# Kernel tuning notes

Measured on AMD Instinct MI355X. Metric: run time of the kernel, lower is better.

## Reference

```python
import jax, jax.numpy as jnp
import numpy as np
from jax import lax

EPS = 1e-5

def conv3x3(x, w):
    # NCHW conv, stride 1, padding 1, no bias
    return lax.conv_general_dilated(x, w, window_strides=(1, 1),
                                    padding=((1, 1), (1, 1)),
                                    dimension_numbers=('NCHW', 'OIHW', 'NCHW'))

def bn_train(x, gamma, beta):
    # training-mode BatchNorm2d: batch stats over (N,H,W), biased variance
    mean = jnp.mean(x, axis=(0, 2, 3), keepdims=True)
    var = jnp.mean((x - mean) ** 2, axis=(0, 2, 3), keepdims=True)
    xn = (x - mean) * lax.rsqrt(var + EPS)
    return xn * gamma[None, :, None, None] + beta[None, :, None, None]

def maxpool2(x):
    return lax.reduce_window(x, -jnp.inf, lax.max, (1, 1, 2, 2), (1, 1, 2, 2), 'VALID')

def decomposed_layer(x, dfe_w, dse_g, dse_b, dse_w, bn_g, bn_b):
    # DFE: conv without bias
    x_dfe = conv3x3(x, dfe_w)                     # [B, T, H, W]
    # DSE vectorized: per-channel BN(1)+ReLU == per-channel BN over T, then
    # 1x1 conv 1->G per channel == scalar expand; concat == interleave (i*G+g)
    xr = jax.nn.relu(bn_train(x_dfe, dse_g, dse_b))
    B, T, H, W = xr.shape
    G = dse_w.shape[1]
    x_dse = jnp.einsum('bihw,ig->bighw', xr, dse_w).reshape(B, T * G, H, W)
    # DFE's BN + ReLU
    return jax.nn.relu(bn_train(x_dse, bn_g, bn_b))

def setup_inputs() -> dict:
    key = jax.random.key(0)
    ks = jax.random.split(key, 12)
    B, G = 4096, 2
    d = {}
    d['x'] = jax.random.normal(ks[0], (B, 3, 32, 32), dtype=jnp.float32)
    # layer 1: T_dfe = ceil(16/2) = 8
    d['dfe1_w'] = jax.random.normal(ks[1], (8, 3, 3, 3), dtype=jnp.float32) * 0.1
    d['dse1_g'] = jnp.ones((8,), jnp.float32)
    d['dse1_b'] = jnp.zeros((8,), jnp.float32)
    d['dse1_w'] = jax.random.normal(ks[2], (8, G), dtype=jnp.float32) * 0.3
    d['bn1_g'] = jnp.ones((16,), jnp.float32)
    d['bn1_b'] = jnp.zeros((16,), jnp.float32)
    # layer 2: T_dfe = ceil(32/2) = 16
    d['dfe2_w'] = jax.random.normal(ks[3], (16, 16, 3, 3), dtype=jnp.float32) * 0.1
    d['dse2_g'] = jnp.ones((16,), jnp.float32)
    d['dse2_b'] = jnp.zeros((16,), jnp.float32)
    d['dse2_w'] = jax.random.normal(ks[4], (16, G), dtype=jnp.float32) * 0.3
    d['bn2_g'] = jnp.ones((32,), jnp.float32)
    d['bn2_b'] = jnp.zeros((32,), jnp.float32)
    # FC head
    d['fc1_w'] = jax.random.normal(ks[5], (512, 32 * 8 * 8), dtype=jnp.float32) * 0.02
    d['fc1_b'] = jnp.zeros((512,), jnp.float32)
    d['fc2_w'] = jax.random.normal(ks[6], (512, 512), dtype=jnp.float32) * 0.04
    d['fc2_b'] = jnp.zeros((512,), jnp.float32)
    d['fc3_w'] = jax.random.normal(ks[7], (10, 512), dtype=jnp.float32) * 0.04
    d['fc3_b'] = jnp.zeros((10,), jnp.float32)
    return d

def reference(x, dfe1_w, dse1_g, dse1_b, dse1_w, bn1_g, bn1_b,
              dfe2_w, dse2_g, dse2_b, dse2_w, bn2_g, bn2_b,
              fc1_w, fc1_b, fc2_w, fc2_b, fc3_w, fc3_b):
    h = decomposed_layer(x, dfe1_w, dse1_g, dse1_b, dse1_w, bn1_g, bn1_b)   # [B,16,32,32]
    h = maxpool2(h)                                                          # [B,16,16,16]
    h = decomposed_layer(h, dfe2_w, dse2_g, dse2_b, dse2_w, bn2_g, bn2_b)   # [B,32,16,16]
    h = maxpool2(h)                                                          # [B,32,8,8]
    h = h.reshape(h.shape[0], -1)                                            # [B,2048]
    h = jax.nn.relu(h @ fc1_w.T + fc1_b)
    h = jax.nn.relu(h @ fc2_w.T + fc2_b)
    return h @ fc3_w.T + fc3_b                                               # [B,10]
```

## Files before the change

kernel.cpp:

```cpp
#include <hip/hip_runtime.h>
#include <math.h>

#define EPS_BN 1e-5

namespace {

constexpr double CNT1 = 4096.0 * 1024.0;
constexpr double CNT2 = 4096.0 * 256.0;

constexpr size_t OFF_Y1 = 0;
constexpr size_t OFF_Y2 = 67108864;
constexpr size_t OFF_H2 = 100663296;
constexpr size_t OFF_A1 = 117440512;
constexpr size_t OFF_A2 = 121634816;
constexpr size_t OFF_ST = 134217728;
constexpr size_t OFF_WB1 = 134283264;
constexpr size_t OFF_WB2 = 136380416;

#define STG(p, i) (p)[(size_t)(i) * 8]

typedef short bf16x8 __attribute__((ext_vector_type(8)));
typedef float f32x4 __attribute__((ext_vector_type(4)));
typedef _Float16 f16;
typedef _Float16 f16x2 __attribute__((ext_vector_type(2)));
typedef _Float16 f16x4 __attribute__((ext_vector_type(4)));
typedef _Float16 f16x8 __attribute__((ext_vector_type(8)));

__device__ __forceinline__ short f2bf(float f) {
  unsigned u = __float_as_uint(f);
  u = (u + 0x7fffu + ((u >> 16) & 1u)) >> 16;
  return (short)u;
}

__device__ __forceinline__ void block_stats_lds(const float* s, const float* q,
                                                float* __restrict__ sred,
                                                double* __restrict__ st) {
  const int tid = threadIdx.x;
#pragma unroll
  for (int j = 0; j < 8; ++j) {
    sred[j * 257 + tid] = s[j];
    sred[(j + 8) * 257 + tid] = q[j];
  }
  __syncthreads();
  const int row = tid >> 4, seg = tid & 15;
  float p = 0.f;
#pragma unroll
  for (int k = 0; k < 16; ++k) {
    const int ke = (k + seg) & 15;
    p += sred[row * 257 + seg * 16 + ke];
  }
  p += __shfl_down(p, 8, 64);
  p += __shfl_down(p, 4, 64);
  p += __shfl_down(p, 2, 64);
  p += __shfl_down(p, 1, 64);
  if (seg == 0) {
    const int c = (row < 8) ? row : row - 8;
    const int slot = (row < 8) ? 2 * c : 2 * c + 1;
    unsafeAtomicAdd(st + (size_t)slot * 8, (double)p);
  }
}

__device__ __forceinline__ float wave_sum(float v) {
#pragma unroll
  for (int o = 32; o > 0; o >>= 1) v += __shfl_down(v, o, 64);
  return v;
}

__global__ __launch_bounds__(256) void k_conv1_y1(
    const float* __restrict__ x, const float* __restrict__ w1,
    f16* __restrict__ y1, double* __restrict__ st1) {
  __shared__ __align__(16) float smem[16 * 257];
  float* xs = smem;
  float* wk = smem + 3672;
  const int tid = threadIdx.x;
  if (tid < 216) wk[(tid % 27) * 8 + tid / 27] = w1[tid];
  const float* xp = x + (size_t)blockIdx.x * 3072;
  for (int i = tid; i < 600; i += 256) {
    const int ci = i / 200, rem = i - ci * 200;
    int r, c;
    if (rem < 36) { r = 0; c = rem; }
    else if (rem < 72) { r = 33; c = rem - 36; }
    else { const int j = rem - 72; r = 1 + (j >> 2); const int m = j & 3;
           c = (m == 0) ? 0 : 32 + m; }
    xs[ci * 1224 + r * 36 + c] = 0.f;
  }
  for (int i = tid; i < 3072; i += 256) {
    const int ci = i >> 10, r = (i >> 5) & 31, c = i & 31;
    xs[ci * 1224 + (r + 1) * 36 + (c + 1)] = xp[i];
  }
  const int rr = tid >> 3, c0 = (tid & 7) * 4;
  __syncthreads();
  float acc[4][8];
#pragma unroll
  for (int p = 0; p < 4; ++p)
#pragma unroll
    for (int co = 0; co < 8; ++co) acc[p][co] = 0.f;
#pragma unroll
  for (int ci = 0; ci < 3; ++ci)
#pragma unroll
    for (int dy = 0; dy < 3; ++dy) {
      const float* rowp = &xs[ci * 1224 + (rr + dy) * 36 + c0];
      float xw[6];
      *(float4*)&xw[0] = *(const float4*)rowp;
      *(float2*)&xw[4] = *(const float2*)(rowp + 4);
#pragma unroll
      for (int dx = 0; dx < 3; ++dx) {
        const int j = ci * 9 + dy * 3 + dx;
        float wv[8];
        *(float4*)&wv[0] = *(const float4*)&wk[j * 8];
        *(float4*)&wv[4] = *(const float4*)&wk[j * 8 + 4];
#pragma unroll
        for (int p = 0; p < 4; ++p)
#pragma unroll
          for (int co = 0; co < 8; ++co) acc[p][co] += xw[p + dx] * wv[co];
      }
    }
  float s[8], q[8];
#pragma unroll
  for (int c = 0; c < 8; ++c) { s[c] = 0.f; q[c] = 0.f; }
  f16* yp = &y1[((size_t)blockIdx.x * 1024 + rr * 32 + c0) * 8];
#pragma unroll
  for (int p = 0; p < 4; ++p) {
    f16 hv8[8];
#pragma unroll
    for (int co = 0; co < 8; ++co) {
      float v = acc[p][co];
      s[co] += v; q[co] += v * v;
      hv8[co] = (f16)v;
    }
    *(uint4*)&yp[p * 8] = *(uint4*)hv8;
  }
  __syncthreads();
  block_stats_lds(s, q, smem, st1 + (size_t)(blockIdx.x & 7) * 128);
}

__global__ __launch_bounds__(256) void k_xr1_stats(
    const f16* __restrict__ y1, const float* __restrict__ g1,
    const float* __restrict__ b1, const double* __restrict__ st1,
    double* __restrict__ st2) {
  __shared__ float sred[16 * 257];
  __shared__ float sA[8], sC[8];
  if (threadIdx.x < 8) {
    const int c = threadIdx.x;
    double sd = 0.0, qd = 0.0;
#pragma unroll
    for (int b = 0; b < 8; ++b) {
      sd += STG(st1, b * 16 + 2 * c);
      qd += STG(st1, b * 16 + 2 * c + 1);
    }
    double md = sd / CNT1;
    float inv = (float)(1.0 / sqrt(qd / CNT1 - md * md + (double)EPS_BN));
    float a = inv * g1[c];
    sA[c] = a;
    sC[c] = b1[c] - (float)md * a;
  }
  __syncthreads();
  float a1[8], c1[8];
#pragma unroll
  for (int c = 0; c < 8; ++c) { a1[c] = sA[c]; c1[c] = sC[c]; }
  const size_t base = (size_t)blockIdx.x * 4096 + threadIdx.x;
  float s[8], q[8];
#pragma unroll
  for (int c = 0; c < 8; ++c) { s[c] = 0.f; q[c] = 0.f; }
#pragma unroll
  for (int k = 0; k < 16; ++k) {
    f16x8 v = *(const f16x8*)&y1[(base + (size_t)k * 256) * 8];
#pragma unroll
    for (int c = 0; c < 8; ++c) {
      float xr = fmaxf((float)v[c] * a1[c] + c1[c], 0.f);
      s[c] += xr; q[c] += xr * xr;
    }
  }
  block_stats_lds(s, q, sred, st2);
}

__global__ __launch_bounds__(256) void k_conv2_fused(
    const f16* __restrict__ y1, const float* __restrict__ g1,
    const float* __restrict__ b1, const float* __restrict__ dsew,
    const float* __restrict__ bng, const float* __restrict__ bnb,
    const float* __restrict__ w2, const double* __restrict__ st1,
    const double* __restrict__ st2, f16* __restrict__ y2,
    double* __restrict__ st3) {
  __shared__ short smem[4 * 5184 + 10 * 256];
  __shared__ float red[4][32];
  __shared__ float cA1[8], cC1[8], cS2[16], cO2[16];
  short* hs = smem;
  short* wt = smem + 4 * 5184;
  const int tid = threadIdx.x, wid = tid >> 6, lane = tid & 63;
  for (int i = tid; i < (4 * 5184 + 10 * 256) / 2; i += 256) ((int*)smem)[i] = 0;
  if (tid < 16) {
    const int i = tid >> 1, g = tid & 1;
    double sd = 0.0, qd = 0.0;
#pragma unroll
    for (int b = 0; b < 8; ++b) {
      sd += STG(st1, b * 16 + 2 * i);
      qd += STG(st1, b * 16 + 2 * i + 1);
    }
    double md = sd / CNT1;
    float inv1 = (float)(1.0 / sqrt(qd / CNT1 - md * md + (double)EPS_BN));
    float a1 = inv1 * g1[i];
    if (g == 0) { cA1[i] = a1; cC1[i] = b1[i] - (float)md * a1; }
    double s2 = STG(st2, 2 * i), q2 = STG(st2, 2 * i + 1);
    double mx = s2 / CNT1, vx = q2 / CNT1 - mx * mx;
    float w = dsew[i * 2 + g];
    double inv2 = 1.0 / sqrt((double)w * w * vx + (double)EPS_BN);
    cS2[tid] = (float)(w * inv2) * bng[tid];
    cO2[tid] = bnb[tid] - (float)(w * mx * inv2) * bng[tid];
  }
  __syncthreads();
  for (int i = tid; i < 2304; i += 256) {
    const int s = i >> 8, co = (i >> 4) & 15, ci = i & 15;
    wt[i] = f2bf(w2[(co * 16 + ci) * 9 + s]);
  }
  const int c = lane & 15, quad = lane >> 4;
  const int ci0 = (quad & 1) * 8;
  int aoff[5];
#pragma unroll
  for (int p = 0; p < 5; ++p) {
    int s = 2 * p + (quad >> 1);
    if (s > 8) s = 8;
    const int dy = s / 3, dx = s % 3;
    aoff[p] = (dy * 18 + (c + dx)) * 16 + ci0;
  }
  float ssum = 0.f, qsum = 0.f;
  const int n0 = blockIdx.x * 4;
  __syncthreads();
  for (int e = tid; e < 2048; e += 256) {
    const int im = e >> 9, j = e & 511, px = j >> 1, half = j & 1;
    const int r = px >> 4, cx = px & 15;
    const size_t pb =
        ((size_t)(n0 + im) * 1024 + (size_t)(2 * r) * 32 + 2 * cx) * 8 +
        half * 4;
    f16x4 vA = *(const f16x4*)&y1[pb];
    f16x4 vB = *(const f16x4*)&y1[pb + 8];
    f16x4 vC = *(const f16x4*)&y1[pb + 256];
    f16x4 vD = *(const f16x4*)&y1[pb + 264];
    short hv[8];
#pragma unroll
    for (int ii = 0; ii < 4; ++ii) {
      const int i = half * 4 + ii;
      float a = cA1[i], cb = cC1[i];
      float x0 = fmaxf((float)vA[ii] * a + cb, 0.f);
      float x1 = fmaxf((float)vB[ii] * a + cb, 0.f);
      float x2 = fmaxf((float)vC[ii] * a + cb, 0.f);
      float x3 = fmaxf((float)vD[ii] * a + cb, 0.f);
#pragma unroll
      for (int g = 0; g < 2; ++g) {
        const int ch = 2 * i + g;
        float sc = cS2[ch], of = cO2[ch];
        float r0 = fmaxf(x0 * sc + of, 0.f);
        float r1 = fmaxf(x1 * sc + of, 0.f);
        float r2 = fmaxf(x2 * sc + of, 0.f);
        float r3 = fmaxf(x3 * sc + of, 0.f);
        hv[ii * 2 + g] = f2bf(fmaxf(fmaxf(r0, r1), fmaxf(r2, r3)));
      }
    }
    *(uint4*)&hs[im * 5184 + ((r + 1) * 18 + (cx + 1)) * 16 + half * 8] =
        *(uint4*)hv;
  }
  __syncthreads();
  bf16x8 bf[5];
#pragma unroll
  for (int p = 0; p < 5; ++p) {
    const int s = 2 * p + (quad >> 1);
    bf[p] = *(const bf16x8*)&wt[s * 256 + c * 16 + ci0];
  }
  const short* hbase = hs + wid * 5184;
  const int img = n0 + wid;
  f16* yp = y2 + ((size_t)img * 16 + c) * 256 + quad * 4;
  for (int r = 0; r < 16; ++r) {
    f32x4 acc = {0.f, 0.f, 0.f, 0.f};
#pragma unroll
    for (int p = 0; p < 5; ++p) {
      bf16x8 a = *(const bf16x8*)&hbase[r * 288 + aoff[p]];
      acc = __builtin_amdgcn_mfma_f32_16x16x32_bf16(a, bf[p], acc, 0, 0, 0);
    }
    f16 hv[4];
#pragma unroll
    for (int g = 0; g < 4; ++g) {
      hv[g] = (f16)acc[g];
      float v = (float)hv[g];
      ssum += v; qsum += v * v;
    }
    *(f16x4*)&yp[r * 16] = *(f16x4*)hv;
  }
  ssum += __shfl_down(ssum, 32, 64); ssum += __shfl_down(ssum, 16, 64);
  qsum += __shfl_down(qsum, 32, 64); qsum += __shfl_down(qsum, 16, 64);
  if (lane < 16) { red[wid][lane] = ssum; red[wid][16 + lane] = qsum; }
  __syncthreads();
  if (tid < 32) {
    const int cc2 = tid & 15, isq = tid >> 4;
    float v = red[0][isq * 16 + cc2] + red[1][isq * 16 + cc2] +
              red[2][isq * 16 + cc2] + red[3][isq * 16 + cc2];
    unsafeAtomicAdd(st3 + (size_t)(2 * cc2 + isq) * 8, (double)v);
  }
}

__global__ __launch_bounds__(256) void k_xr2_stats(
    const f16* __restrict__ y2, const float* __restrict__ g2,
    const float* __restrict__ b2, const double* __restrict__ st3,
    double* __restrict__ st4) {
  __shared__ float red[32];
  const int tid = threadIdx.x, c = tid >> 4, seg = tid & 15;
  double sd = STG(st3, 2 * c), qd = STG(st3, 2 * c + 1);
  double md = sd / CNT2;
  float inv = (float)(1.0 / sqrt(qd / CNT2 - md * md + (double)EPS_BN));
  float a3 = inv * g2[c];
  float c3 = b2[c] - (float)md * a3;
  float s = 0.f, q = 0.f;
#pragma unroll
  for (int k = 0; k < 8; ++k) {
    const f16* p =
        &y2[(((size_t)(blockIdx.x * 8 + k)) * 16 + c) * 256 + seg * 16];
    f16x8 v0 = *(const f16x8*)p;
    f16x8 v1 = *(const f16x8*)(p + 8);
#pragma unroll
    for (int j = 0; j < 8; ++j) {
      float x0 = fmaxf((float)v0[j] * a3 + c3, 0.f);
      float x1 = fmaxf((float)v1[j] * a3 + c3, 0.f);
      s += x0 + x1; q += x0 * x0 + x1 * x1;
    }
  }
#pragma unroll
  for (int o = 8; o > 0; o >>= 1) {
    s += __shfl_down(s, o, 64);
    q += __shfl_down(q, o, 64);
  }
  if ((tid & 15) == 0) { red[2 * c] = s; red[2 * c + 1] = q; }
  __syncthreads();
  if (tid < 32) unsafeAtomicAdd(st4 + (size_t)tid * 8, (double)red[tid]);
}

__global__ __launch_bounds__(256) void k_l2_out(
    const f16* __restrict__ y2, const float* __restrict__ g2,
    const float* __restrict__ b2, const float* __restrict__ dsew,
    const float* __restrict__ bng, const float* __restrict__ bnb,
    const double* __restrict__ st3, const double* __restrict__ st4,
    short* __restrict__ h2) {
  __shared__ float cS3[16], cO3[16], cS4[32], cO4[32];
  const int tid = threadIdx.x;
  if (tid < 32) {
    const int i = tid >> 1, g = tid & 1;
    double sd = STG(st3, 2 * i), qd = STG(st3, 2 * i + 1);
    double md = sd / CNT2;
    float inv3 = (float)(1.0 / sqrt(qd / CNT2 - md * md + (double)EPS_BN));
    float a3 = inv3 * g2[i];
    if (g == 0) { cS3[i] = a3; cO3[i] = b2[i] - (float)md * a3; }
    double s4 = STG(st4, 2 * i), q4 = STG(st4, 2 * i + 1);
    double mx = s4 / CNT2, vx = q4 / CNT2 - mx * mx;
    float w = dsew[2 * i + g];
    double inv4 = 1.0 / sqrt((double)w * w * vx + (double)EPS_BN);
    cS4[tid] = (float)(w * inv4) * bng[tid];
    cO4[tid] = bnb[tid] - (float)(w * mx * inv4) * bng[tid];
  }
  __syncthreads();
  const int sub = tid >> 6, lane = tid & 63;
  const int n = blockIdx.x * 4 + sub;
  const int px = lane & 7, py = lane >> 3;
#pragma unroll
  for (int i = 0; i < 16; ++i) {
    const size_t base = ((size_t)n * 16 + i) * 256;
    f16x2 v01 = *(const f16x2*)&y2[base + (2 * py) * 16 + 2 * px];
    f16x2 v23 = *(const f16x2*)&y2[base + (2 * py + 1) * 16 + 2 * px];
    float a3 = cS3[i], c3 = cO3[i];
    float xr0 = fmaxf((float)v01[0] * a3 + c3, 0.f);
    float xr1 = fmaxf((float)v01[1] * a3 + c3, 0.f);
    float xr2 = fmaxf((float)v23[0] * a3 + c3, 0.f);
    float xr3 = fmaxf((float)v23[1] * a3 + c3, 0.f);
#pragma unroll
    for (int g = 0; g < 2; ++g) {
      const int c = 2 * i + g;
      float sc = cS4[c], of = cO4[c];
      float r0 = fmaxf(xr0 * sc + of, 0.f);
      float r1 = fmaxf(xr1 * sc + of, 0.f);
      float r2 = fmaxf(xr2 * sc + of, 0.f);
      float r3 = fmaxf(xr3 * sc + of, 0.f);
      h2[(size_t)n * 2048 + c * 64 + py * 8 + px] =
          f2bf(fmaxf(fmaxf(r0, r1), fmaxf(r2, r3)));
    }
  }
}

__global__ __launch_bounds__(256) void k_cast_w(const float* __restrict__ w1,
                                                const float* __restrict__ w2,
                                                short* __restrict__ o1,
                                                short* __restrict__ o2,
                                                double* __restrict__ st) {
  const int i4 = blockIdx.x * 256 + threadIdx.x;
  if (blockIdx.x == 0) {
    for (int k = threadIdx.x; k < 1664; k += 256) st[k] = 0.0;
  }
  if (i4 < 262144) {
    float4 v = ((const float4*)w1)[i4];
    short h[4] = {f2bf(v.x), f2bf(v.y), f2bf(v.z), f2bf(v.w)};
    ((uint2*)o1)[i4] = *(uint2*)h;
  } else if (i4 < 327680) {
    const int j = i4 - 262144;
    float4 v = ((const float4*)w2)[j];
    short h[4] = {f2bf(v.x), f2bf(v.y), f2bf(v.z), f2bf(v.w)};
    ((uint2*)o2)[j] = *(uint2*)h;
  }
}

template <int K, int RELU, int OUT_BF16>
__global__ __launch_bounds__(256) void k_fc_lds(
    const short* __restrict__ A, const short* __restrict__ W,
    const float* __restrict__ bias, void* __restrict__ Cv) {
  __shared__ __align__(16) short lds[2][2][64 * 64];
  const int tid = threadIdx.x, w = tid >> 6, lane = tid & 63;
  const int id = blockIdx.y * 8 + blockIdx.x;
  const int bx = (id >> 3) & 7;
  const int by = ((id >> 6) << 3) | (id & 7);
  const int bm = by * 64, bn = bx * 64;
  const int cl = lane & 15, quad = lane >> 4;
  const int srow = lane >> 3, sseg = lane & 7;
  const size_t soff = (size_t)srow * K + ((size_t)(sseg ^ srow) << 3);
  const short* aS0 = A + (size_t)(bm + w * 16) * K + soff;
  const short* aS1 = A + (size_t)(bm + w * 16 + 8) * K + soff;
  const short* bS0 = W + (size_t)(bn + w * 16) * K + soff;
  const short* bS1 = W + (size_t)(bn + w * 16 + 8) * K + soff;

#define GLD16(src, dst)                                                    \
  __builtin_amdgcn_global_load_lds(                                        \
      (const __attribute__((address_space(1))) void*)(const void*)(src),   \
      (__attribute__((address_space(3))) void*)(void*)(dst), 16, 0, 0)
#define STAGE(buf, k0)                                               \
  do {                                                               \
    GLD16(aS0 + (k0), &lds[buf][0][(w * 16) * 64]);                  \
    GLD16(aS1 + (k0), &lds[buf][0][(w * 16 + 8) * 64]);              \
    GLD16(bS0 + (k0), &lds[buf][1][(w * 16) * 64]);                  \
    GLD16(bS1 + (k0), &lds[buf][1][(w * 16 + 8) * 64]);              \
  } while (0)

  f32x4 acc[4];
#pragma unroll
  for (int ct = 0; ct < 4; ++ct) acc[ct] = (f32x4){0.f, 0.f, 0.f, 0.f};
  int aOff[2], bOff0[2];
#pragma unroll
  for (int kk = 0; kk < 2; ++kk) {
    const int sw = ((kk * 4 + quad) ^ (cl & 7)) << 3;
    aOff[kk] = (w * 16 + cl) * 64 + sw;
    bOff0[kk] = cl * 64 + sw;
  }
  constexpr int NT = K / 64;
  STAGE(0, 0);
#pragma unroll 2
  for (int t = 0; t < NT; ++t) {
    asm volatile("s_waitcnt vmcnt(0)" ::: "memory");
    __syncthreads();
    if (t + 1 < NT) STAGE((t + 1) & 1, (t + 1) * 64);
    const short* As = &lds[t & 1][0][0];
    const short* Bs = &lds[t & 1][1][0];
#pragma unroll
    for (int kk = 0; kk < 2; ++kk) {
      bf16x8 a = *(const bf16x8*)&As[aOff[kk]];
#pragma unroll
      for (int ct = 0; ct < 4; ++ct) {
        bf16x8 b = *(const bf16x8*)&Bs[bOff0[kk] + ct * 1024];
        acc[ct] = __builtin_amdgcn_mfma_f32_16x16x32_bf16(a, b, acc[ct], 0, 0, 0);
      }
    }
  }
#undef STAGE
#undef GLD16
#pragma unroll
  for (int ct = 0; ct < 4; ++ct) {
    const int col = bn + ct * 16 + cl;
    const float bia = bias[col];
#pragma unroll
    for (int r = 0; r < 4; ++r) {
      const int row = bm + w * 16 + quad * 4 + r;
      float v = acc[ct][r] + bia;
      if (RELU) v = fmaxf(v, 0.f);
      if (OUT_BF16)
        ((short*)Cv)[(size_t)row * 512 + col] = f2bf(v);
      else
        ((float*)Cv)[(size_t)row * 512 + col] = v;
    }
  }
}

__global__ __launch_bounds__(256) void k_fc3(const float* __restrict__ A,
                                             const float* __restrict__ W,
                                             const float* __restrict__ b,
                                             float* __restrict__ out) {
  const int wid = threadIdx.x >> 6, lane = threadIdx.x & 63;
  const int row = blockIdx.x * 4 + wid;
  float p[10];
#pragma unroll
  for (int o = 0; o < 10; ++o) p[o] = 0.f;
  const float* a = A + (size_t)row * 512;
#pragma unroll
  for (int jj = 0; jj < 8; ++jj) {
    const int j = lane + jj * 64;
    float av = a[j];
#pragma unroll
    for (int o = 0; o < 10; ++o) p[o] += av * W[o * 512 + j];
  }
#pragma unroll
  for (int o = 0; o < 10; ++o) p[o] = wave_sum(p[o]);
  if (lane == 0) {
#pragma unroll
    for (int o = 0; o < 10; ++o) out[(size_t)row * 10 + o] = p[o] + b[o];
  }
}

}

extern "C" void kernel_launch(void* const* d_in, const int* in_sizes, int n_in,
                              void* d_out, int out_size, void* d_ws,
                              size_t ws_size, hipStream_t stream) {
  const float* x      = (const float*)d_in[0];
  const float* dfe1_w = (const float*)d_in[1];
  const float* dse1_g = (const float*)d_in[2];
  const float* dse1_b = (const float*)d_in[3];
  const float* dse1_w = (const float*)d_in[4];
  const float* bn1_g  = (const float*)d_in[5];
  const float* bn1_b  = (const float*)d_in[6];
  const float* dfe2_w = (const float*)d_in[7];
  const float* dse2_g = (const float*)d_in[8];
  const float* dse2_b = (const float*)d_in[9];
  const float* dse2_w = (const float*)d_in[10];
  const float* bn2_g  = (const float*)d_in[11];
  const float* bn2_b  = (const float*)d_in[12];
  const float* fc1_w  = (const float*)d_in[13];
  const float* fc1_b  = (const float*)d_in[14];
  const float* fc2_w  = (const float*)d_in[15];
  const float* fc2_b  = (const float*)d_in[16];
  const float* fc3_w  = (const float*)d_in[17];
  const float* fc3_b  = (const float*)d_in[18];
  float* out = (float*)d_out;
  char* ws = (char*)d_ws;
  f16* y1 = (f16*)(ws + OFF_Y1);
  f16* y2 = (f16*)(ws + OFF_Y2);
  short* h2 = (short*)(ws + OFF_H2);
  short* a1 = (short*)(ws + OFF_A1);
  float* a2 = (float*)(ws + OFF_A2);
  short* wb1 = (short*)(ws + OFF_WB1);
  short* wb2 = (short*)(ws + OFF_WB2);
  double* st = (double*)(ws + OFF_ST);
  double* ST1 = st;
  double* ST2 = st + (size_t)128 * 8;
  double* ST3 = st + (size_t)144 * 8;
  double* ST4 = st + (size_t)176 * 8;

  k_cast_w<<<1280, 256, 0, stream>>>(fc1_w, fc2_w, wb1, wb2, st);
  k_conv1_y1<<<4096, 256, 0, stream>>>(x, dfe1_w, y1, ST1);
  k_xr1_stats<<<1024, 256, 0, stream>>>(y1, dse1_g, dse1_b, ST1, ST2);
  k_conv2_fused<<<1024, 256, 0, stream>>>(y1, dse1_g, dse1_b, dse1_w, bn1_g,
                                          bn1_b, dfe2_w, ST1, ST2, y2, ST3);
  k_xr2_stats<<<512, 256, 0, stream>>>(y2, dse2_g, dse2_b, ST3, ST4);
  k_l2_out<<<1024, 256, 0, stream>>>(y2, dse2_g, dse2_b, dse2_w, bn2_g, bn2_b,
                                     ST3, ST4, h2);
  k_fc_lds<2048, 1, 1><<<dim3(8, 64), 256, 0, stream>>>(h2, wb1, fc1_b, a1);
  k_fc_lds<512, 1, 0><<<dim3(8, 64), 256, 0, stream>>>(a1, wb2, fc2_b, a2);
  k_fc3<<<1024, 256, 0, stream>>>(a2, fc3_w, fc3_b, out);
}
```

Measured before the change: 293.2 us.

## Rewrite conv1 as row-streaming per-image warp kernel with shuffles

The first 3x3 conv no longer stages a padded image tile in LDS. Each 32-lane group now owns one image and streams rows through registers, using lane shuffles for horizontal neighbours and three rotating accumulators for vertical taps. The weight transpose moves into the cast kernel, and the launch shrinks from one block per image to one block per 8 images. This removes the LDS fill, its barriers and the per-block weight reshuffle, but cuts the grid to 512 blocks and serialises 32 row steps per thread, with weights read from global/L1 each step.

```diff
diff --git a/kernel.cpp b/kernel.cpp
--- a/kernel.cpp
+++ b/kernel.cpp
@@ -14,6 +14,7 @@
 constexpr size_t OFF_A1 = 117440512;
 constexpr size_t OFF_A2 = 121634816;
 constexpr size_t OFF_ST = 134217728;
+constexpr size_t OFF_WT = 134234112;
 constexpr size_t OFF_WB1 = 134283264;
 constexpr size_t OFF_WB2 = 136380416;
 
@@ -67,71 +68,75 @@
 }
 
 __global__ __launch_bounds__(256) void k_conv1_y1(
-    const float* __restrict__ x, const float* __restrict__ w1,
+    const float* __restrict__ x, const float* __restrict__ wt,
     f16* __restrict__ y1, double* __restrict__ st1) {
-  __shared__ __align__(16) float smem[16 * 257];
-  float* xs = smem;
-  float* wk = smem + 3672;
+  __shared__ float sred[16 * 257];
   const int tid = threadIdx.x;
-  if (tid < 216) wk[(tid % 27) * 8 + tid / 27] = w1[tid];
-  const float* xp = x + (size_t)blockIdx.x * 3072;
-  for (int i = tid; i < 600; i += 256) {
-    const int ci = i / 200, rem = i - ci * 200;
-    int r, c;
-    if (rem < 36) { r = 0; c = rem; }
-    else if (rem < 72) { r = 33; c = rem - 36; }
-    else { const int j = rem - 72; r = 1 + (j >> 2); const int m = j & 3;
-           c = (m == 0) ? 0 : 32 + m; }
-    xs[ci * 1224 + r * 36 + c] = 0.f;
-  }
-  for (int i = tid; i < 3072; i += 256) {
-    const int ci = i >> 10, r = (i >> 5) & 31, c = i & 31;
-    xs[ci * 1224 + (r + 1) * 36 + (c + 1)] = xp[i];
-  }
-  const int rr = tid >> 3, c0 = (tid & 7) * 4;
-  __syncthreads();
-  float acc[4][8];
-#pragma unroll
-  for (int p = 0; p < 4; ++p)
-#pragma unroll
-    for (int co = 0; co < 8; ++co) acc[p][co] = 0.f;
-#pragma unroll
-  for (int ci = 0; ci < 3; ++ci)
-#pragma unroll
-    for (int dy = 0; dy < 3; ++dy) {
-      const float* rowp = &xs[ci * 1224 + (rr + dy) * 36 + c0];
-      float xw[6];
-      *(float4*)&xw[0] = *(const float4*)rowp;
-      *(float2*)&xw[4] = *(const float2*)(rowp + 4);
-#pragma unroll
-      for (int dx = 0; dx < 3; ++dx) {
-        const int j = ci * 9 + dy * 3 + dx;
-        float wv[8];
-        *(float4*)&wv[0] = *(const float4*)&wk[j * 8];
-        *(float4*)&wv[4] = *(const float4*)&wk[j * 8 + 4];
-#pragma unroll
-        for (int p = 0; p < 4; ++p)
-#pragma unroll
-          for (int co = 0; co < 8; ++co) acc[p][co] += xw[p + dx] * wv[co];
-      }
-    }
-  float s[8], q[8];
-#pragma unroll
-  for (int c = 0; c < 8; ++c) { s[c] = 0.f; q[c] = 0.f; }
-  f16* yp = &y1[((size_t)blockIdx.x * 1024 + rr * 32 + c0) * 8];
-#pragma unroll
-  for (int p = 0; p < 4; ++p) {
-    f16 hv8[8];
-#pragma unroll
-    for (int co = 0; co < 8; ++co) {
-      float v = acc[p][co];
-      s[co] += v; q[co] += v * v;
-      hv8[co] = (f16)v;
-    }
-    *(uint4*)&yp[p * 8] = *(uint4*)hv8;
-  }
-  __syncthreads();
-  block_stats_lds(s, q, smem, st1 + (size_t)(blockIdx.x & 7) * 128);
+  const int img = tid >> 5, c = tid & 31;
+  const int n = blockIdx.x * 8 + img;
+  const float* xp = x + (size_t)n * 3072 + c;
+  f16* yp = y1 + (size_t)n * 8192;
+  float a0[8], a1[8], a2[8], s[8], q[8];
+#pragma unroll
+  for (int co = 0; co < 8; ++co) {
+    a0[co] = 0.f; a1[co] = 0.f; a2[co] = 0.f; s[co] = 0.f; q[co] = 0.f;
+  }
+  float xM[3];
+  xM[0] = xp[0]; xM[1] = xp[1024]; xM[2] = xp[2048];
+
+#define CONTRIB(ACC, T, XV)                                           \
+  {                                                                   \
+    const float4 wa = *(const float4*)&wt[(T) * 8];                   \
+    const float4 wb = *(const float4*)&wt[(T) * 8 + 4];               \
+    ACC[0] += wa.x * (XV); ACC[1] += wa.y * (XV);                     \
+    ACC[2] += wa.z * (XV); ACC[3] += wa.w * (XV);                     \
+    ACC[4] += wb.x * (XV); ACC[5] += wb.y * (XV);                     \
+    ACC[6] += wb.z * (XV); ACC[7] += wb.w * (XV);                     \
+  }
+
+#define STEP(R, AP, AC, AN)                                           \
+  {                                                                   \
+    float nM0 = 0.f, nM1 = 0.f, nM2 = 0.f;                            \
+    if ((R) <= 30) {                                                  \
+      const float* rp = xp + ((R) + 1) * 32;                          \
+      nM0 = rp[0]; nM1 = rp[1024]; nM2 = rp[2048];                    \
+    }                                                                 \
+    _Pragma("unroll") for (int ci = 0; ci < 3; ++ci) {                \
+      const float xm = xM[ci];                                        \
+      float xl = __shfl_up(xm, 1, 64);                                \
+      float xr = __shfl_down(xm, 1, 64);                              \
+      if (c == 0) xl = 0.f;                                           \
+      if (c == 31) xr = 0.f;                                          \
+      CONTRIB(AN, ci * 9 + 0, xl);                                    \
+      CONTRIB(AN, ci * 9 + 1, xm);                                    \
+      CONTRIB(AN, ci * 9 + 2, xr);                                    \
+      CONTRIB(AC, ci * 9 + 3, xl);                                    \
+      CONTRIB(AC, ci * 9 + 4, xm);                                    \
+      CONTRIB(AC, ci * 9 + 5, xr);                                    \
+      CONTRIB(AP, ci * 9 + 6, xl);                                    \
+      CONTRIB(AP, ci * 9 + 7, xm);                                    \
+      CONTRIB(AP, ci * 9 + 8, xr);                                    \
+    }                                                                 \
+    if ((R) >= 1) {                                                   \
+      f16 hv[8];                                                      \
+      _Pragma("unroll") for (int co = 0; co < 8; ++co) {              \
+        float v = AP[co];                                             \
+        s[co] += v; q[co] += v * v; hv[co] = (f16)v;                  \
+      }                                                               \
+      *(uint4*)&yp[(size_t)((R) - 1) * 256 + c * 8] = *(uint4*)hv;    \
+    }                                                                 \
+    _Pragma("unroll") for (int co = 0; co < 8; ++co) AP[co] = 0.f;    \
+    xM[0] = nM0; xM[1] = nM1; xM[2] = nM2;                            \
+  }
+
+  for (int rb = 0; rb < 33; rb += 3) {
+    STEP(rb,     a2, a0, a1);
+    STEP(rb + 1, a0, a1, a2);
+    STEP(rb + 2, a1, a2, a0);
+  }
+#undef STEP
+#undef CONTRIB
+  block_stats_lds(s, q, sred, st1 + (size_t)(blockIdx.x & 7) * 128);
 }
 
 __global__ __launch_bounds__(256) void k_xr1_stats(
@@ -383,12 +388,16 @@
 
 __global__ __launch_bounds__(256) void k_cast_w(const float* __restrict__ w1,
                                                 const float* __restrict__ w2,
+                                                const float* __restrict__ dfe1,
                                                 short* __restrict__ o1,
                                                 short* __restrict__ o2,
-                                                double* __restrict__ st) {
+                                                double* __restrict__ st,
+                                                float* __restrict__ wt) {
   const int i4 = blockIdx.x * 256 + threadIdx.x;
   if (blockIdx.x == 0) {
     for (int k = threadIdx.x; k < 1664; k += 256) st[k] = 0.0;
+    if (threadIdx.x < 216)
+      wt[(threadIdx.x % 27) * 8 + threadIdx.x / 27] = dfe1[threadIdx.x];
   }
   if (i4 < 262144) {
     float4 v = ((const float4*)w1)[i4];
@@ -538,14 +547,15 @@
   float* a2 = (float*)(ws + OFF_A2);
   short* wb1 = (short*)(ws + OFF_WB1);
   short* wb2 = (short*)(ws + OFF_WB2);
+  float* wt1 = (float*)(ws + OFF_WT);
   double* st = (double*)(ws + OFF_ST);
   double* ST1 = st;
   double* ST2 = st + (size_t)128 * 8;
   double* ST3 = st + (size_t)144 * 8;
   double* ST4 = st + (size_t)176 * 8;
 
-  k_cast_w<<<1280, 256, 0, stream>>>(fc1_w, fc2_w, wb1, wb2, st);
-  k_conv1_y1<<<4096, 256, 0, stream>>>(x, dfe1_w, y1, ST1);
+  k_cast_w<<<1280, 256, 0, stream>>>(fc1_w, fc2_w, dfe1_w, wb1, wb2, st, wt1);
+  k_conv1_y1<<<512, 256, 0, stream>>>(x, wt1, y1, ST1);
   k_xr1_stats<<<1024, 256, 0, stream>>>(y1, dse1_g, dse1_b, ST1, ST2);
   k_conv2_fused<<<1024, 256, 0, stream>>>(y1, dse1_g, dse1_b, dse1_w, bn1_g,
                                           bn1_b, dfe2_w, ST1, ST2, y2, ST3);
```

Measured after the change: 296.7 us. Within noise of the previous version (+1.2%).
